# Optimization experiments

Measured on AMD Instinct MI355X. Metric: run time of the kernel, lower is better.

## Reference

```python
import jax, jax.numpy as jnp
import numpy as np

B, S, D, H = 1, 4096, 1024, 16
HD = D // H  # 64
THETA = 10000.0


def precompute_freqs_cis(dim, end, theta=THETA):
    freqs = 1.0 / theta ** (np.arange(0, dim, 2, dtype=np.float32) / dim)  # [dim//2]
    t = np.arange(end, dtype=np.float32)
    f = np.outer(t, freqs)                       # [end, dim//2]
    f = np.concatenate((f, f), axis=-1)          # [end, dim]
    return jnp.asarray(np.cos(f), jnp.float32), jnp.asarray(np.sin(f), jnp.float32)


def rotate_half(x):
    x1 = x[..., : x.shape[-1] // 2]
    x2 = x[..., x.shape[-1] // 2:]
    return jnp.concatenate((-x2, x1), axis=-1)


def setup_inputs() -> dict:
    key = jax.random.key(0)
    ks = jax.random.split(key, 5)
    x = jax.random.normal(ks[0], (B, S, D), jnp.float32)
    scale = 0.02
    Wq = jax.random.normal(ks[1], (D, H, HD), jnp.float32) * scale
    Wk = jax.random.normal(ks[2], (D, H, HD), jnp.float32) * scale
    Wv = jax.random.normal(ks[3], (D, H, HD), jnp.float32) * scale
    Wo = jax.random.normal(ks[4], (H, HD, D), jnp.float32) * scale
    mask = jnp.tril(jnp.ones((S, S), jnp.bool_))[None, None]  # [1,1,S,S] causal
    return {"x": x, "mask": mask, "Wq": Wq, "Wk": Wk, "Wv": Wv, "Wo": Wo}


def reference(x, mask, Wq, Wk, Wv, Wo):
    # QKV projections: [B,S,D] x [D,H,HD] -> [B,S,H,HD]
    q = jnp.einsum('bsd,dhe->bshe', x, Wq)
    k = jnp.einsum('bsd,dhe->bshe', x, Wk)
    v = jnp.einsum('bsd,dhe->bshe', x, Wv)
    # Rotary position embedding
    cos, sin = precompute_freqs_cis(HD, S)
    cos = cos[None, :, None, :]  # [1,S,1,HD]
    sin = sin[None, :, None, :]
    q = q * cos + rotate_half(q) * sin
    k = k * cos + rotate_half(k) * sin
    # Scaled dot-product attention
    scale = 1.0 / jnp.sqrt(jnp.asarray(HD, jnp.float32))
    scores = jnp.einsum('bqhe,bkhe->bhqk', q * scale, k)  # [B,H,S,S]
    big_neg = jnp.finfo(scores.dtype).min
    scores = jnp.where(mask, scores, big_neg)
    attn = jax.nn.softmax(scores, axis=-1)
    ctx = jnp.einsum('bhqk,bkhe->bqhe', attn, v)  # [B,S,H,HD]
    # Output projection contracting (head, head_dim)
    out = jnp.einsum('bqhe,hed->bqd', ctx, Wo)  # [B,S,D]
    return out
```

## Files before the change

kernel.cpp:

```cpp
#include <hip/hip_runtime.h>
#include <hip/hip_bf16.h>
#include <stdint.h>
#include <stddef.h>

#define S_LEN 4096
#define DMODEL 1024
#define NHEAD 16
#define HDIM 64
#define L2E 1.4426950408889634f
#define FIXED_M 8.0f

typedef __attribute__((ext_vector_type(8))) short bf16x8;
typedef __attribute__((ext_vector_type(8))) unsigned short u16x8;
typedef __attribute__((ext_vector_type(4))) float f32x4;
typedef __attribute__((ext_vector_type(16))) float f32x16;

__device__ __forceinline__ unsigned short f2bf(float f) {
    unsigned int u = __float_as_uint(f);
    return (unsigned short)((u + 0x7FFFu + ((u >> 16) & 1u)) >> 16);
}
__device__ __forceinline__ float bf2f(unsigned short h) {
    return __uint_as_float(((unsigned int)h) << 16);
}

__device__ __forceinline__ void gload_lds16(const unsigned short* g, unsigned short* l) {
    __builtin_amdgcn_global_load_lds(
        (const __attribute__((address_space(1))) unsigned int*)g,
        (__attribute__((address_space(3))) unsigned int*)l, 16, 0, 0);
}

__global__ __launch_bounds__(256) void prep_kernel(
    const float* __restrict__ x,
    const float* __restrict__ w0, const float* __restrict__ w1,
    const float* __restrict__ w2, const float* __restrict__ w3,
    unsigned short* __restrict__ xb,
    unsigned short* __restrict__ t0, unsigned short* __restrict__ t1,
    unsigned short* __restrict__ t2, unsigned short* __restrict__ t3,
    float* __restrict__ ctab, float* __restrict__ stab) {
    int bid = blockIdx.x;
    int t = threadIdx.x;
    if (bid < 1024) {
        const float* src; unsigned short* dst;
        switch (bid >> 8) {
            case 0: src = w0; dst = t0; break;
            case 1: src = w1; dst = t1; break;
            case 2: src = w2; dst = t2; break;
            default: src = w3; dst = t3; break;
        }
        __shared__ float tile[64][65];
        int k0 = ((bid >> 4) & 15) * 64, n0 = (bid & 15) * 64;
        int r = t >> 2, q4 = (t & 3) * 16;
        const float* sp = src + (size_t)(k0 + r) * DMODEL + n0 + q4;
        #pragma unroll
        for (int j = 0; j < 4; ++j) {
            f32x4 v = *(const f32x4*)(sp + j * 4);
            #pragma unroll
            for (int e = 0; e < 4; ++e) tile[r][q4 + j * 4 + e] = v[e];
        }
        __syncthreads();
        int n = t >> 2, kq = (t & 3) * 16;
        unsigned short* dp = dst + (size_t)(n0 + n) * DMODEL + k0 + kq;
        u16x8 a, b;
        #pragma unroll
        for (int j = 0; j < 8; ++j) { a[j] = f2bf(tile[kq + j][n]); b[j] = f2bf(tile[kq + 8 + j][n]); }
        *(u16x8*)dp = a;
        *(u16x8*)(dp + 8) = b;
    } else if (bid < 3072) {
        int i = ((bid - 1024) * 256 + t) * 8;
        f32x4 a = *(const f32x4*)(x + i);
        f32x4 b = *(const f32x4*)(x + i + 4);
        u16x8 o;
        #pragma unroll
        for (int j = 0; j < 4; ++j) { o[j] = f2bf(a[j]); o[4 + j] = f2bf(b[j]); }
        *(u16x8*)(xb + i) = o;
    } else {
        int i = (bid - 3072) * 256 + t;
        int s = i >> 5, j = i & 31;
        float freq = exp2f(-0.41524101186092407f * (float)j);
        float ang = (float)s * freq;
        ctab[i] = cosf(ang);
        stab[i] = sinf(ang);
    }
}

template<int MODE>
__global__ __launch_bounds__(256) void gemm_kernel(
    const unsigned short* __restrict__ Ab,
    const unsigned short* __restrict__ B0,
    const unsigned short* __restrict__ B1,
    const unsigned short* __restrict__ B2,
    unsigned short* __restrict__ o0,
    unsigned short* __restrict__ o1,
    unsigned short* __restrict__ o2,
    float* __restrict__ fo,
    const float* __restrict__ ctab,
    const float* __restrict__ stab) {
    int z = blockIdx.z;
    const unsigned short* Bt = (MODE == 0) ? B0 : (z == 0 ? B0 : (z == 1 ? B1 : B2));
    unsigned short* outp     = (MODE == 0) ? o0 : (z == 0 ? o0 : (z == 1 ? o1 : o2));
    int m0 = blockIdx.y * 128, n0 = blockIdx.x * 128;
    __shared__ unsigned short As[128][64];
    __shared__ unsigned short Bs[128][64];
    int t = threadIdx.x, w = t >> 6, l = t & 63;
    int wm = w >> 1, wn = w & 1, g = l >> 4, c = l & 15;

    f32x4 acc[4][4];
    #pragma unroll
    for (int m = 0; m < 4; ++m)
        #pragma unroll
        for (int n = 0; n < 4; ++n) acc[m][n] = (f32x4){0.f, 0.f, 0.f, 0.f};

    int srow8 = l >> 3;
    int scs = (l & 7) ^ srow8;

    for (int kt = 0; kt < DMODEL; kt += 64) {
        __syncthreads();
        #pragma unroll
        for (int ch = 0; ch < 4; ++ch) {
            int qd = w * 4 + ch;
            gload_lds16(Ab + (size_t)(m0 + qd * 8 + srow8) * DMODEL + kt + scs * 8,
                        (unsigned short*)As + qd * 512);
            gload_lds16(Bt + (size_t)(n0 + qd * 8 + srow8) * DMODEL + kt + scs * 8,
                        (unsigned short*)Bs + qd * 512);
        }
        __syncthreads();
        #pragma unroll
        for (int kk = 0; kk < 64; kk += 32) {
            bf16x8 af[4], bf[4];
            #pragma unroll
            for (int m = 0; m < 4; ++m) {
                int ra = wm * 64 + m * 16 + c;
                af[m] = *(const bf16x8*)&As[ra][(((kk >> 3) + g) ^ (ra & 7)) << 3];
            }
            #pragma unroll
            for (int n = 0; n < 4; ++n) {
                int rb = wn * 64 + n * 16 + c;
                bf[n] = *(const bf16x8*)&Bs[rb][(((kk >> 3) + g) ^ (rb & 7)) << 3];
            }
            #pragma unroll
            for (int m = 0; m < 4; ++m)
                #pragma unroll
                for (int n = 0; n < 4; ++n)
                    acc[m][n] = __builtin_amdgcn_mfma_f32_16x16x32_bf16(af[m], bf[n], acc[m][n], 0, 0, 0);
        }
    }

    if (MODE == 1 && z < 2) {
        float sc8 = (z == 0) ? 0.125f * L2E : 1.0f;
        #pragma unroll
        for (int m = 0; m < 4; ++m) {
            #pragma unroll
            for (int r = 0; r < 4; ++r) {
                int srow = m0 + wm * 64 + m * 16 + g * 4 + r;
                #pragma unroll
                for (int n = 0; n < 2; ++n) {
                    int e = n * 16 + c;
                    float cs = ctab[srow * 32 + e];
                    float sn = stab[srow * 32 + e];
                    float lo = acc[m][n][r], hi = acc[m][n + 2][r];
                    float nlo = (lo * cs - hi * sn) * sc8;
                    float nhi = (hi * cs + lo * sn) * sc8;
                    size_t base = (size_t)srow * DMODEL + n0 + wn * 64;
                    outp[base + n * 16 + c]       = f2bf(nlo);
                    outp[base + (n + 2) * 16 + c] = f2bf(nhi);
                }
            }
        }
    } else if (MODE == 1) {
        #pragma unroll
        for (int m = 0; m < 4; ++m)
            #pragma unroll
            for (int r = 0; r < 4; ++r) {
                int srow = m0 + wm * 64 + m * 16 + g * 4 + r;
                size_t base = (size_t)srow * DMODEL + n0 + wn * 64;
                #pragma unroll
                for (int n = 0; n < 4; ++n)
                    outp[base + n * 16 + c] = f2bf(acc[m][n][r]);
            }
    } else {
        #pragma unroll
        for (int m = 0; m < 4; ++m)
            #pragma unroll
            for (int r = 0; r < 4; ++r) {
                int srow = m0 + wm * 64 + m * 16 + g * 4 + r;
                size_t base = (size_t)srow * DMODEL + n0 + wn * 64;
                #pragma unroll
                for (int n = 0; n < 4; ++n)
                    fo[base + n * 16 + c] = acc[m][n][r];
            }
    }
}

__global__ __launch_bounds__(512, 4) void attn_kernel(
    const unsigned short* __restrict__ q,
    const unsigned short* __restrict__ k,
    const unsigned short* __restrict__ v,
    unsigned short* __restrict__ ctx,
    unsigned short* __restrict__ Opart,
    float* __restrict__ lpart) {
    int h = blockIdx.x;
    int pair = blockIdx.y;
    int p = blockIdx.z;
    int t = threadIdx.x, w = t >> 6, l = t & 63, c = l & 31, hi = l >> 5;
    int rg = w & 3, ks = w >> 2;

    __shared__ __align__(16) char smraw[36864];
    unsigned short (*KsT)[64][72] = (unsigned short (*)[64][72])smraw;
    unsigned short (*VtT)[64][72] = (unsigned short (*)[64][72])(smraw + 18432);
    float (*Om2)[66] = (float (*)[66])smraw;
    float* ml2       = (float*)(smraw + 33792);

    int ts = t & 255;
    int skr = ts >> 2, skc = (ts & 3) * 16;
    int svr = ts & 63, svc = ((ts >> 6) & 3) * 16;
    int svp = (svr & ~0xC) | ((svr & 4) << 1) | ((svr & 8) >> 1);
    const unsigned short* gkb = k + (size_t)skr * DMODEL + h * HDIM + skc;
    const unsigned short* gvb = v + (size_t)svr * DMODEL + h * HDIM + svc;

    auto run_segment = [&](int qb, int t0, int cnt, bool finalize) {
        int qrow = qb * 128 + rg * 32 + c;
        int wrmax = qb * 128 + rg * 32 + 31;

        bf16x8 qf[4];
        {
            const unsigned short* qp = q + (size_t)qrow * DMODEL + h * HDIM + hi * 8;
            #pragma unroll
            for (int s = 0; s < 4; ++s) qf[s] = *(const bf16x8*)(qp + s * 16);
        }
        f32x16 o0, o1;
        #pragma unroll
        for (int i = 0; i < 16; ++i) { o0[i] = 0.f; o1[i] = 0.f; }
        float lsum = 0.f;

        u16x8 ka, kb, va, vb;
        if (ks < cnt) {
            size_t off = (size_t)((t0 + ks) * 64) * DMODEL;
            ka = *(const u16x8*)(gkb + off);
            kb = *(const u16x8*)(gkb + off + 8);
            va = *(const u16x8*)(gvb + off);
            vb = *(const u16x8*)(gvb + off + 8);
            *(u16x8*)&KsT[ks][skr][skc]     = ka;
            *(u16x8*)&KsT[ks][skr][skc + 8] = kb;
            #pragma unroll
            for (int j = 0; j < 8; ++j) {
                VtT[ks][svc + j][svp]     = va[j];
                VtT[ks][svc + 8 + j][svp] = vb[j];
            }
        }

        int NIT = (cnt + 1) >> 1;
        for (int it = 0; it < NIT; ++it) {
            int j = 2 * it + ks;
            int kv0 = (t0 + j) * 64;
            if (j + 2 < cnt) {
                size_t off = (size_t)(kv0 + 128) * DMODEL;
                ka = *(const u16x8*)(gkb + off);
                kb = *(const u16x8*)(gkb + off + 8);
                va = *(const u16x8*)(gvb + off);
                vb = *(const u16x8*)(gvb + off + 8);
            }
            __syncthreads();

            if (j < cnt) {
                #pragma unroll
                for (int h2 = 0; h2 < 2; ++h2) {
                    int kbase = kv0 + h2 * 32;
                    if (kbase > wrmax) continue;

                    f32x16 sf;
                    #pragma unroll
                    for (int i = 0; i < 16; ++i) sf[i] = 0.f;
                    __builtin_amdgcn_s_setprio(1);
                    #pragma unroll
                    for (int s = 0; s < 4; ++s) {
                        bf16x8 kf = *(const bf16x8*)&KsT[ks][h2 * 32 + c][s * 16 + hi * 8];
                        sf = __builtin_amdgcn_mfma_f32_32x32x16_bf16(kf, qf[s], sf, 0, 0, 0);
                    }
                    __builtin_amdgcn_s_setprio(0);

                    if (kbase + 31 >= wrmax) {
                        #pragma unroll
                        for (int r = 0; r < 16; ++r) {
                            int key = kbase + (r & 3) + 8 * (r >> 2) + 4 * hi;
                            if (key > qrow) sf[r] = -3.0e38f;
                        }
                    }

                    float ps = 0.f;
                    union { unsigned int u[8]; bf16x8 v[2]; } pu;
                    #pragma unroll
                    for (int jj = 0; jj < 8; ++jj) {
                        float p0 = exp2f(sf[2 * jj]     - FIXED_M);
                        float p1 = exp2f(sf[2 * jj + 1] - FIXED_M);
                        ps += p0 + p1;
                        union { struct { __hip_bfloat16 x, y; } hh; unsigned int u; } cv;
                        cv.hh.x = __float2bfloat16(p0);
                        cv.hh.y = __float2bfloat16(p1);
                        pu.u[jj] = cv.u;
                    }
                    lsum += ps;

                    __builtin_amdgcn_s_setprio(1);
                    {
                        bf16x8 a00 = *(const bf16x8*)&VtT[ks][c][h2 * 32 + hi * 8];
                        bf16x8 a01 = *(const bf16x8*)&VtT[ks][c][h2 * 32 + 16 + hi * 8];
                        bf16x8 a10 = *(const bf16x8*)&VtT[ks][32 + c][h2 * 32 + hi * 8];
                        bf16x8 a11 = *(const bf16x8*)&VtT[ks][32 + c][h2 * 32 + 16 + hi * 8];
                        o0 = __builtin_amdgcn_mfma_f32_32x32x16_bf16(a00, pu.v[0], o0, 0, 0, 0);
                        o0 = __builtin_amdgcn_mfma_f32_32x32x16_bf16(a01, pu.v[1], o0, 0, 0, 0);
                        o1 = __builtin_amdgcn_mfma_f32_32x32x16_bf16(a10, pu.v[0], o1, 0, 0, 0);
                        o1 = __builtin_amdgcn_mfma_f32_32x32x16_bf16(a11, pu.v[1], o1, 0, 0, 0);
                    }
                    __builtin_amdgcn_s_setprio(0);
                }
            }

            if (it + 1 < NIT) {
                __syncthreads();
                if (j + 2 < cnt) {
                    *(u16x8*)&KsT[ks][skr][skc]     = ka;
                    *(u16x8*)&KsT[ks][skr][skc + 8] = kb;
                    #pragma unroll
                    for (int jj = 0; jj < 8; ++jj) {
                        VtT[ks][svc + jj][svp]     = va[jj];
                        VtT[ks][svc + 8 + jj][svp] = vb[jj];
                    }
                }
            }
        }

        lsum += __shfl_xor(lsum, 32, 64);

        __syncthreads();
        if (ks == 0) {
            #pragma unroll
            for (int r = 0; r < 16; ++r) {
                int dim = (r & 3) + 8 * (r >> 2) + 4 * hi;
                Om2[rg * 32 + c][dim]      = o0[r];
                Om2[rg * 32 + c][dim + 32] = o1[r];
            }
            if (hi == 0) ml2[rg * 32 + c] = lsum;
        }
        __syncthreads();
        if (ks == 1) {
            float lc = ml2[rg * 32 + c] + lsum;
            float sc = finalize ? 1.0f / lc : 1.0f;
            #pragma unroll
            for (int r = 0; r < 16; ++r) {
                int dim = (r & 3) + 8 * (r >> 2) + 4 * hi;
                Om2[rg * 32 + c][dim]      = (Om2[rg * 32 + c][dim]      + o0[r]) * sc;
                Om2[rg * 32 + c][dim + 32] = (Om2[rg * 32 + c][dim + 32] + o1[r]) * sc;
            }
            if (!finalize && hi == 0)
                lpart[(size_t)(p * 16 + h) * 4096 + qrow] = lc;
        }
        __syncthreads();
        {
            int row = t >> 2, d0 = (t & 3) * 16;
            u16x8 oa, ob;
            #pragma unroll
            for (int j = 0; j < 8; ++j) {
                oa[j] = f2bf(Om2[row][d0 + j]);
                ob[j] = f2bf(Om2[row][d0 + 8 + j]);
            }
            if (finalize) {
                size_t cb = (size_t)(qb * 128 + row) * DMODEL + h * HDIM + d0;
                *(u16x8*)&ctx[cb]     = oa;
                *(u16x8*)&ctx[cb + 8] = ob;
            } else {
                size_t obase = ((size_t)(p * 16 + h) * 4096 + qb * 128 + row) * 64 + d0;
                *(u16x8*)&Opart[obase]     = oa;
                *(u16x8*)&Opart[obase + 8] = ob;
            }
        }
        __syncthreads();
    };

    if (p == 0) {
        run_segment(pair, 0, 2 * pair + 2, true);
        run_segment(31 - pair, 0, 31 - 2 * pair, false);
    } else {
        run_segment(31 - pair, 31 - 2 * pair, 33, false);
    }
}

__global__ __launch_bounds__(256) void attn_merge_kernel(
    const unsigned short* __restrict__ Op,
    const float* __restrict__ lp,
    unsigned short* __restrict__ ctx) {
    int i = blockIdx.x * 256 + threadIdx.x;
    int g8 = i & 7;
    int row = 2048 + ((i >> 3) & 2047);
    int h = i >> 14;
    size_t idx = (size_t)h * 4096 + row;
    const size_t PS = (size_t)16 * 4096;
    float inv = 1.0f / (lp[idx] + lp[PS + idx]);
    u16x8 v0 = *(const u16x8*)(Op + idx * 64 + g8 * 8);
    u16x8 v1 = *(const u16x8*)(Op + (PS + idx) * 64 + g8 * 8);
    u16x8 o;
    #pragma unroll
    for (int j = 0; j < 8; ++j)
        o[j] = f2bf((bf2f(v0[j]) + bf2f(v1[j])) * inv);
    *(u16x8*)(ctx + (size_t)row * DMODEL + h * 64 + g8 * 8) = o;
}

extern "C" void kernel_launch(void* const* d_in, const int* in_sizes, int n_in,
                              void* d_out, int out_size, void* d_ws, size_t ws_size,
                              hipStream_t stream) {
    const float* x  = (const float*)d_in[0];
    const float* Wq = (const float*)d_in[2];
    const float* Wk = (const float*)d_in[3];
    const float* Wv = (const float*)d_in[4];
    const float* Wo = (const float*)d_in[5];

    char* ws = (char*)d_ws;
    float* ctab = (float*)(ws);
    float* stab = (float*)(ws + (512u << 10));
    unsigned short* ctx = (unsigned short*)(ws + (1u  << 20));
    unsigned short* Wtq = (unsigned short*)(ws + (1u  << 20));
    unsigned short* Wtk = (unsigned short*)(ws + (3u  << 20));
    unsigned short* Wtv = (unsigned short*)(ws + (5u  << 20));
    unsigned short* Wto = (unsigned short*)(ws + (9u  << 20));
    unsigned short* kr  = (unsigned short*)(ws + (11u << 20));
    unsigned short* vb  = (unsigned short*)(ws + (19u << 20));
    unsigned short* qr  = (unsigned short*)(ws + (27u << 20));
    unsigned short* xb  = (unsigned short*)(ws + (35u << 20));
    unsigned short* Opart = (unsigned short*)(ws + (43u << 20));
    float* lpart = (float*)(ws + (59u << 20));

    prep_kernel<<<3584, 256, 0, stream>>>(x, Wq, Wk, Wv, Wo, xb,
                                          Wtq, Wtk, Wtv, Wto, ctab, stab);
    gemm_kernel<1><<<dim3(8, 32, 3), 256, 0, stream>>>(xb, Wtq, Wtk, Wtv,
                                                       qr, kr, vb, nullptr, ctab, stab);
    attn_kernel<<<dim3(16, 16, 2), 512, 0, stream>>>(qr, kr, vb, ctx, Opart, lpart);
    attn_merge_kernel<<<(16 * 2048 * 8) / 256, 256, 0, stream>>>(Opart, lpart, ctx);
    gemm_kernel<0><<<dim3(8, 32, 1), 256, 0, stream>>>(ctx, Wto, nullptr, nullptr,
                                                       nullptr, nullptr, nullptr,
                                                       (float*)d_out, ctab, stab);
}
```

Measured before the change: 151.3 us.

## Split attention KV loop across four wave groups per block

Attention blocks grow from 512 to 1024 threads, so four KV-split wave groups (instead of two) each process every fourth 64-key tile, with double the shared memory for K/V tiles. The partial outputs and row sums are reduced serially through shared memory in three stages, and normalization moves into the final bf16 store loop. This is meant to raise per-block parallelism and latency hiding on the causal attention. In exchange it costs more barriers in the reduction, halves the resident blocks per CU (launch bounds 1024,2 with 72KB LDS), and shrinks per-wave work on short causal segments.

```diff
diff --git a/kernel.cpp b/kernel.cpp
--- a/kernel.cpp
+++ b/kernel.cpp
@@ -191,7 +191,7 @@
     }
 }
 
-__global__ __launch_bounds__(512, 4) void attn_kernel(
+__global__ __launch_bounds__(1024, 2) void attn_kernel(
     const unsigned short* __restrict__ q,
     const unsigned short* __restrict__ k,
     const unsigned short* __restrict__ v,
@@ -204,9 +204,9 @@
     int t = threadIdx.x, w = t >> 6, l = t & 63, c = l & 31, hi = l >> 5;
     int rg = w & 3, ks = w >> 2;
 
-    __shared__ __align__(16) char smraw[36864];
+    __shared__ __align__(16) char smraw[73728];
     unsigned short (*KsT)[64][72] = (unsigned short (*)[64][72])smraw;
-    unsigned short (*VtT)[64][72] = (unsigned short (*)[64][72])(smraw + 18432);
+    unsigned short (*VtT)[64][72] = (unsigned short (*)[64][72])(smraw + 36864);
     float (*Om2)[66] = (float (*)[66])smraw;
     float* ml2       = (float*)(smraw + 33792);
 
@@ -248,12 +248,12 @@
             }
         }
 
-        int NIT = (cnt + 1) >> 1;
+        int NIT = (cnt + 3) >> 2;
         for (int it = 0; it < NIT; ++it) {
-            int j = 2 * it + ks;
+            int j = 4 * it + ks;
             int kv0 = (t0 + j) * 64;
-            if (j + 2 < cnt) {
-                size_t off = (size_t)(kv0 + 128) * DMODEL;
+            if (j + 4 < cnt) {
+                size_t off = (size_t)(kv0 + 256) * DMODEL;
                 ka = *(const u16x8*)(gkb + off);
                 kb = *(const u16x8*)(gkb + off + 8);
                 va = *(const u16x8*)(gvb + off);
@@ -317,7 +317,7 @@
 
             if (it + 1 < NIT) {
                 __syncthreads();
-                if (j + 2 < cnt) {
+                if (j + 4 < cnt) {
                     *(u16x8*)&KsT[ks][skr][skc]     = ka;
                     *(u16x8*)&KsT[ks][skr][skc + 8] = kb;
                     #pragma unroll
@@ -343,34 +343,53 @@
         }
         __syncthreads();
         if (ks == 1) {
-            float lc = ml2[rg * 32 + c] + lsum;
-            float sc = finalize ? 1.0f / lc : 1.0f;
             #pragma unroll
             for (int r = 0; r < 16; ++r) {
                 int dim = (r & 3) + 8 * (r >> 2) + 4 * hi;
-                Om2[rg * 32 + c][dim]      = (Om2[rg * 32 + c][dim]      + o0[r]) * sc;
-                Om2[rg * 32 + c][dim + 32] = (Om2[rg * 32 + c][dim + 32] + o1[r]) * sc;
-            }
-            if (!finalize && hi == 0)
-                lpart[(size_t)(p * 16 + h) * 4096 + qrow] = lc;
+                Om2[rg * 32 + c][dim]      += o0[r];
+                Om2[rg * 32 + c][dim + 32] += o1[r];
+            }
+            if (hi == 0) ml2[rg * 32 + c] += lsum;
+        }
+        __syncthreads();
+        if (ks == 2) {
+            #pragma unroll
+            for (int r = 0; r < 16; ++r) {
+                int dim = (r & 3) + 8 * (r >> 2) + 4 * hi;
+                Om2[rg * 32 + c][dim]      += o0[r];
+                Om2[rg * 32 + c][dim + 32] += o1[r];
+            }
+            if (hi == 0) ml2[rg * 32 + c] += lsum;
+        }
+        __syncthreads();
+        if (ks == 3) {
+            #pragma unroll
+            for (int r = 0; r < 16; ++r) {
+                int dim = (r & 3) + 8 * (r >> 2) + 4 * hi;
+                Om2[rg * 32 + c][dim]      += o0[r];
+                Om2[rg * 32 + c][dim + 32] += o1[r];
+            }
+            if (hi == 0) {
+                float lc = ml2[rg * 32 + c] + lsum;
+                ml2[rg * 32 + c] = finalize ? 1.0f / lc : 1.0f;
+                if (!finalize)
+                    lpart[(size_t)(p * 16 + h) * 4096 + qrow] = lc;
+            }
         }
         __syncthreads();
         {
-            int row = t >> 2, d0 = (t & 3) * 16;
-            u16x8 oa, ob;
-            #pragma unroll
-            for (int j = 0; j < 8; ++j) {
-                oa[j] = f2bf(Om2[row][d0 + j]);
-                ob[j] = f2bf(Om2[row][d0 + 8 + j]);
-            }
+            int row = t >> 3, d0 = (t & 7) * 8;
+            float sc = ml2[row];
+            u16x8 oa;
+            #pragma unroll
+            for (int j = 0; j < 8; ++j)
+                oa[j] = f2bf(Om2[row][d0 + j] * sc);
             if (finalize) {
                 size_t cb = (size_t)(qb * 128 + row) * DMODEL + h * HDIM + d0;
-                *(u16x8*)&ctx[cb]     = oa;
-                *(u16x8*)&ctx[cb + 8] = ob;
+                *(u16x8*)&ctx[cb] = oa;
             } else {
                 size_t obase = ((size_t)(p * 16 + h) * 4096 + qb * 128 + row) * 64 + d0;
-                *(u16x8*)&Opart[obase]     = oa;
-                *(u16x8*)&Opart[obase + 8] = ob;
+                *(u16x8*)&Opart[obase] = oa;
             }
         }
         __syncthreads();
@@ -432,7 +451,7 @@
                                           Wtq, Wtk, Wtv, Wto, ctab, stab);
     gemm_kernel<1><<<dim3(8, 32, 3), 256, 0, stream>>>(xb, Wtq, Wtk, Wtv,
                                                        qr, kr, vb, nullptr, ctab, stab);
-    attn_kernel<<<dim3(16, 16, 2), 512, 0, stream>>>(qr, kr, vb, ctx, Opart, lpart);
+    attn_kernel<<<dim3(16, 16, 2), 1024, 0, stream>>>(qr, kr, vb, ctx, Opart, lpart);
     attn_merge_kernel<<<(16 * 2048 * 8) / 256, 256, 0, stream>>>(Opart, lpart, ctx);
     gemm_kernel<0><<<dim3(8, 32, 1), 256, 0, stream>>>(ctx, Wto, nullptr, nullptr,
                                                        nullptr, nullptr, nullptr,
```

Result: slower. 165.2 us (+9.2%).
